# Kernel optimization log

Measured on AMD Instinct MI355X. Metric: run time of the kernel, lower is better.

The kernel has to match this reference:

```python
import jax, jax.numpy as jnp
import numpy as np

EPS = 1e-5
GROUPS = 32


def conv2d(x, w, b):
    # x: [N,C,H,W], w: [O,I,3,3] (or 1x1), stride 1, padding 'same' for 3x3
    kh = w.shape[2]
    pad = (kh - 1) // 2
    y = jax.lax.conv_general_dilated(x, w, (1, 1), ((pad, pad), (pad, pad)),
                                     dimension_numbers=('NCHW', 'OIHW', 'NCHW'))
    return y + b[None, :, None, None]


def group_norm(x, g, b):
    N, C, H, W = x.shape
    xr = x.reshape(N, GROUPS, C // GROUPS, H, W)
    mu = xr.mean(axis=(2, 3, 4), keepdims=True)
    var = xr.var(axis=(2, 3, 4), keepdims=True)
    xr = (xr - mu) / jnp.sqrt(var + EPS)
    return xr.reshape(N, C, H, W) * g[None, :, None, None] + b[None, :, None, None]


def batch_norm(x, g, b):
    # training-mode BatchNorm2d: batch statistics over (N,H,W)
    mu = x.mean(axis=(0, 2, 3), keepdims=True)
    var = x.var(axis=(0, 2, 3), keepdims=True)
    return (x - mu) / jnp.sqrt(var + EPS) * g[None, :, None, None] + b[None, :, None, None]


def binary_activation(x):
    # STE: forward sign(x), backward through piecewise poly out3
    out_fwd = jnp.sign(x)
    m1 = (x < -1).astype(x.dtype)
    m2 = (x < 0).astype(x.dtype)
    m3 = (x < 1).astype(x.dtype)
    out1 = -1.0 * m1 + (x * x + 2.0 * x) * (1.0 - m1)
    out2 = out1 * m2 + (-x * x + 2.0 * x) * (1.0 - m2)
    out3 = out2 * m3 + 1.0 * (1.0 - m3)
    return jax.lax.stop_gradient(out_fwd - out3) + out3


def hard_binary_conv(x, w, b):
    # per-output-channel scaling * sign(w), STE through clipped weights
    scale = jax.lax.stop_gradient(jnp.mean(jnp.abs(w), axis=(1, 2, 3), keepdims=True))
    bw_ng = scale * jnp.sign(w)
    clipped = jnp.clip(w, -1.0, 1.0)
    bw = jax.lax.stop_gradient(bw_ng - clipped) + clipped
    return conv2d(x, bw, b)


def learnable_bias(x, emb, w, b):
    bias = jax.nn.silu(emb) @ w.T + b  # [B, C]
    return x + bias[:, :, None, None]


def _forward(c, x, emb,
             rb_gn1_g, rb_gn1_b, rb_conv1_w, rb_conv1_b, rb_emb_w, rb_emb_b,
             rb_gn2_g, rb_gn2_b, rb_conv2_w, rb_conv2_b,
             m1_w, m1_b, bconv_w, bconv_b, bn_g, bn_b,
             m2_w, m2_b, prelu_a, m3_w, m3_b):
    # ResBlock (skip = Identity since out_channels == channels)
    h = conv2d(jax.nn.silu(group_norm(c, rb_gn1_g, rb_gn1_b)), rb_conv1_w, rb_conv1_b)
    eo = jax.nn.silu(emb) @ rb_emb_w.T + rb_emb_b          # [B, 2*C]
    scale, shift = jnp.split(eo[:, :, None, None], 2, axis=1)
    h = group_norm(h, rb_gn2_g, rb_gn2_b) * (1.0 + scale) + shift
    h = conv2d(jax.nn.silu(h), rb_conv2_w, rb_conv2_b)
    c2 = c + h
    # concat + bias + STE binarize + binary conv + BN + channel-pool residual + PReLU
    xc = jnp.concatenate([x, c2], axis=1)                   # [B, 2C, H, W]
    out = learnable_bias(xc, emb, m1_w, m1_b)
    out = binary_activation(out)
    out = hard_binary_conv(out, bconv_w, bconv_b)
    out = batch_norm(out, bn_g, bn_b)
    N, C2, H, W = xc.shape
    out = out + xc.reshape(N, C2 // 2, 2, H, W).mean(axis=2)  # channel mean pooling
    out = learnable_bias(out, emb, m2_w, m2_b)
    out = jnp.where(out >= 0, out, prelu_a[None, :, None, None] * out)  # PReLU
    out = learnable_bias(out, emb, m3_w, m3_b)
    return out


def setup_inputs() -> dict:
    key = jax.random.key(0)
    ks = jax.random.split(key, 24)
    B, C, EMB, H, W = 8, 128, 512, 64, 64
    IN2 = 2 * C
    n = lambda k, s, sc=0.05: jax.random.normal(k, s, dtype=jnp.float32) * sc
    return {
        'c': jax.random.normal(ks[0], (B, C, H, W), dtype=jnp.float32),
        'x': jax.random.normal(ks[1], (B, C, H, W), dtype=jnp.float32),
        'emb': jax.random.normal(ks[2], (B, EMB), dtype=jnp.float32),
        'rb_gn1_g': jnp.ones((C,), jnp.float32), 'rb_gn1_b': jnp.zeros((C,), jnp.float32),
        'rb_conv1_w': n(ks[3], (C, C, 3, 3)), 'rb_conv1_b': n(ks[4], (C,)),
        'rb_emb_w': n(ks[5], (2 * C, EMB)), 'rb_emb_b': n(ks[6], (2 * C,)),
        'rb_gn2_g': jnp.ones((C,), jnp.float32), 'rb_gn2_b': jnp.zeros((C,), jnp.float32),
        'rb_conv2_w': n(ks[7], (C, C, 3, 3)), 'rb_conv2_b': n(ks[8], (C,)),
        'm1_w': n(ks[9], (IN2, EMB)), 'm1_b': n(ks[10], (IN2,)),
        'bconv_w': jax.random.uniform(ks[11], (C, IN2, 3, 3), dtype=jnp.float32) * 0.001,
        'bconv_b': n(ks[12], (C,)),
        'bn_g': jnp.ones((C,), jnp.float32), 'bn_b': jnp.zeros((C,), jnp.float32),
        'm2_w': n(ks[13], (C, EMB)), 'm2_b': n(ks[14], (C,)),
        'prelu_a': jnp.full((C,), 0.25, jnp.float32),
        'm3_w': n(ks[15], (C, EMB)), 'm3_b': n(ks[16], (C,)),
    }


def reference(c, x, emb,
              rb_gn1_g, rb_gn1_b, rb_conv1_w, rb_conv1_b, rb_emb_w, rb_emb_b,
              rb_gn2_g, rb_gn2_b, rb_conv2_w, rb_conv2_b,
              m1_w, m1_b, bconv_w, bconv_b, bn_g, bn_b,
              m2_w, m2_b, prelu_a, m3_w, m3_b):
    return _forward(c, x, emb,
                    rb_gn1_g, rb_gn1_b, rb_conv1_w, rb_conv1_b, rb_emb_w, rb_emb_b,
                    rb_gn2_g, rb_gn2_b, rb_conv2_w, rb_conv2_b,
                    m1_w, m1_b, bconv_w, bconv_b, bn_g, bn_b,
                    m2_w, m2_b, prelu_a, m3_w, m3_b)
```

## Files before the change

### kernel.cpp

```cpp
#include <hip/hip_runtime.h>
#include <stdint.h>


#define B_   8
#define C_   128
#define C2_  256
#define HW_  4096
#define EMB_ 512
#define EPS_ 1e-5f

typedef int   v16i __attribute__((ext_vector_type(16)));
typedef float v16f __attribute__((ext_vector_type(16)));
typedef short v8s  __attribute__((ext_vector_type(8)));
typedef int   v4i  __attribute__((ext_vector_type(4)));

#define COLB 272
#define LDSZ (3 * 66 * COLB)
#define TSTRIDE 132

__device__ __forceinline__ float silu(float v) {
    return v * __builtin_amdgcn_rcpf(1.f + __expf(-v));
}
__device__ __forceinline__ unsigned short f2bf(float f) {
    unsigned int x = __float_as_uint(f);
    return (unsigned short)((x + 0x7FFFu + ((x >> 16) & 1u)) >> 16);
}
__device__ __forceinline__ int8_t sgn8(float v) {
    return (v > 0.f) ? (int8_t)1 : ((v < 0.f) ? (int8_t)(-1) : (int8_t)0);
}

__device__ __forceinline__ void stage_one(char* lds, int r, const char* src) {
    const int tid = threadIdx.x;
#pragma unroll
    for (int it = 0; it < 4; ++it) {
        int idx = it * 256 + tid;
        int x = idx >> 4, o = idx & 15;
        char* dst = lds + (r * 66 + x + 1) * COLB + o * 16;
        if (src) *(float4*)dst = *(const float4*)(src + x * 256 + o * 16);
        else     *(float4*)dst = make_float4(0.f, 0.f, 0.f, 0.f);
    }
}
__device__ __forceinline__ void stage3(char* lds, const char* r0,
                                       const char* r1, const char* r2) {
    const int tid = threadIdx.x;
    if (tid < 96) {
        int r = tid / 32, q = tid & 31;
        int c = (q >> 4) ? 65 : 0, o = q & 15;
        *(float4*)(lds + (r * 66 + c) * COLB + o * 16) = make_float4(0.f, 0.f, 0.f, 0.f);
    }
    stage_one(lds, 0, r0);
    stage_one(lds, 1, r1);
    stage_one(lds, 2, r2);
}

__global__ __launch_bounds__(256) void k_prep(
    const float* __restrict__ w, int8_t* __restrict__ sgn,
    float* __restrict__ alpha, float* __restrict__ bnS, float* __restrict__ bnQ,
    float* __restrict__ gnS, float* __restrict__ gnQ,
    const float* __restrict__ w1, const float* __restrict__ w2,
    unsigned short* __restrict__ Wc1, unsigned short* __restrict__ Wc2,
    const float* __restrict__ emb,
    const float* __restrict__ ew, const float* __restrict__ ebb,
    const float* __restrict__ m1w, const float* __restrict__ m1b,
    const float* __restrict__ m2w, const float* __restrict__ m2b,
    const float* __restrict__ m3w, const float* __restrict__ m3b,
    float* __restrict__ eo, float* __restrict__ b1,
    float* __restrict__ b2, float* __restrict__ b3,
    const float* __restrict__ gin, const float* __restrict__ g1w,
    const float* __restrict__ g1b, unsigned short* __restrict__ act1) {
    __shared__ float red[256];
    const int blk = blockIdx.x, tid = threadIdx.x;
    if (blk < 128) {
        const int o = blk;
        if (o == 0 && tid < 128) { bnS[tid] = 0.f; bnQ[tid] = 0.f; }
        if (o == 1) { gnS[tid] = 0.f; }
        if (o == 2) { gnQ[tid] = 0.f; }
        const float* wr = w + (size_t)o * (C2_ * 9);
        float s = 0.f;
        for (int i = tid; i < C2_ * 9; i += 256) s += fabsf(wr[i]);
        red[tid] = s;
        __syncthreads();
        for (int st = 128; st > 0; st >>= 1) {
            if (tid < st) red[tid] += red[tid + st];
            __syncthreads();
        }
        if (tid == 0) alpha[o] = red[0] / (float)(C2_ * 9);
        for (int kk = 0; kk < 9; ++kk) {
            float v = wr[tid * 9 + kk];
            sgn[((size_t)(kk * 16 + (tid >> 4)) * C_ + o) * 16 + (tid & 15)] = sgn8(v);
        }
    } else if (blk < 704) {
        int i = (blk - 128) * 256 + tid;
        int co = i / (C_ * 9);
        int rem = i - co * (C_ * 9);
        int ci = rem / 9, kk = rem - ci * 9;
        size_t d = ((size_t)(kk * 16 + (ci >> 3)) * C_ + co) * 8 + (ci & 7);
        Wc1[d] = f2bf(w1[i]);
        Wc2[d] = f2bf(w2[i]);
    } else if (blk < 896) {
        const int o = (blk - 704) * 4 + (tid >> 6);
        const int l = tid & 63;
        const float* wv;
        float bias;
        float* dst;
        int dstride;
        if (o < 256)      { wv = ew  + (size_t)o * EMB_;              bias = ebb[o];    dst = eo + o;  dstride = 256; }
        else if (o < 512) { int r = o - 256; wv = m1w + (size_t)r * EMB_; bias = m1b[r]; dst = b1 + r; dstride = 256; }
        else if (o < 640) { int r = o - 512; wv = m2w + (size_t)r * EMB_; bias = m2b[r]; dst = b2 + r; dstride = 128; }
        else              { int r = o - 640; wv = m3w + (size_t)r * EMB_; bias = m3b[r]; dst = b3 + r; dstride = 128; }
        const float4 wa = *(const float4*)(wv + 8 * l);
        const float4 wb = *(const float4*)(wv + 8 * l + 4);
#pragma unroll
        for (int b = 0; b < B_; ++b) {
            const float* s = emb + b * EMB_ + 8 * l;
            float4 sa = *(const float4*)(s);
            float4 sb = *(const float4*)(s + 4);
            float p = wa.x * silu(sa.x) + wa.y * silu(sa.y) + wa.z * silu(sa.z) + wa.w * silu(sa.w) +
                      wb.x * silu(sb.x) + wb.y * silu(sb.y) + wb.z * silu(sb.z) + wb.w * silu(sb.w);
#pragma unroll
            for (int off = 32; off > 0; off >>= 1) p += __shfl_down(p, off, 64);
            if (l == 0) dst[b * dstride] = bias + p;
        }
    } else {
        const int bb = blk - 896;
        const int n = bb >> 5, grp = bb & 31;
        const size_t base = ((size_t)(n * C_ + grp * 4)) << 12;
        float sum = 0.f, sq = 0.f;
        const float4* in4 = (const float4*)(gin + base);
        for (int i = tid; i < 4096; i += 256) {
            float4 v = in4[i];
            sum += v.x + v.y + v.z + v.w;
            sq += v.x * v.x + v.y * v.y + v.z * v.z + v.w * v.w;
        }
#pragma unroll
        for (int off = 32; off > 0; off >>= 1) {
            sum += __shfl_xor(sum, off, 64);
            sq  += __shfl_xor(sq, off, 64);
        }
        if ((tid & 63) == 0) { red[tid >> 6] = sum; red[8 + (tid >> 6)] = sq; }
        __syncthreads();
        sum = red[0] + red[1] + red[2] + red[3];
        sq  = red[8] + red[9] + red[10] + red[11];
        const float mu = sum * (1.f / 16384.f);
        const float rstd = rsqrtf(sq * (1.f / 16384.f) - mu * mu + EPS_);
        float gg[4], bb4[4];
#pragma unroll
        for (int j = 0; j < 4; ++j) { gg[j] = g1w[grp * 4 + j]; bb4[j] = g1b[grp * 4 + j]; }
        union F4 { float4 v; float f[4]; };
        for (int i = tid; i < 1024; i += 256) {
            const int hw = 4 * i;
            F4 vj[4];
#pragma unroll
            for (int j = 0; j < 4; ++j)
                vj[j].v = *(const float4*)(gin + base + ((size_t)j << 12) + hw);
#pragma unroll
            for (int e = 0; e < 4; ++e) {
                union { unsigned short u[4]; uint2 v; } pk;
#pragma unroll
                for (int j = 0; j < 4; ++j)
                    pk.u[j] = f2bf(silu((vj[j].f[e] - mu) * rstd * gg[j] + bb4[j]));
                *(uint2*)(act1 + ((size_t)(n * HW_ + hw + e)) * C_ + grp * 4) = pk.v;
            }
        }
    }
}

__global__ __launch_bounds__(256) void k_conv1(const unsigned short* __restrict__ act,
                                               const unsigned short* __restrict__ Wc,
                                               const float* __restrict__ bias,
                                               float* __restrict__ outN,
                                               float* __restrict__ gnS,
                                               float* __restrict__ gnQ) {
    __shared__ __align__(16) char lds[LDSZ];
    const int y = blockIdx.x;
    const int n = blockIdx.y;
    const char* base = (const char*)(act + ((size_t)n * 64) * 64 * C_);
    stage3(lds,
           (y > 0)  ? base + (size_t)(y - 1) * 16384 : nullptr,
           base + (size_t)y * 16384,
           (y < 63) ? base + (size_t)(y + 1) * 16384 : nullptr);
    __syncthreads();

    const int w = threadIdx.x >> 6;
    const int l = threadIdx.x & 63;
    const int lm = l & 31;
    const int lh = l >> 5;

    v16f acc0, acc1;
#pragma unroll
    for (int i = 0; i < 16; ++i) { acc0[i] = 0.f; acc1[i] = 0.f; }

#pragma unroll
    for (int kk = 0; kk < 9; ++kk) {
        const int r = kk / 3, dx = kk % 3 - 1;
        const char* col0 = lds + (r * 66 + lm + 1 + dx) * COLB + 16 * lh;
        const char* col1 = col0 + 32 * COLB;
        const unsigned short* wbase = Wc + (size_t)(kk * 16 + lh) * C_ * 8 + (32 * w + lm) * 8;
#pragma unroll
        for (int cb = 0; cb < 8; ++cb) {
            v8s a = *(const v8s*)(wbase + (size_t)(2 * cb) * C_ * 8);
            v8s b0 = *(const v8s*)(col0 + 32 * cb);
            v8s b1 = *(const v8s*)(col1 + 32 * cb);
            acc0 = __builtin_amdgcn_mfma_f32_32x32x16_bf16(a, b0, acc0, 0, 0, 0);
            acc1 = __builtin_amdgcn_mfma_f32_32x32x16_bf16(a, b1, acc1, 0, 0, 0);
        }
    }
    float sv0[16], sv1[16], pr[16], qr[16];
#pragma unroll
    for (int r = 0; r < 16; ++r) {
        const int row = (r & 3) + 8 * (r >> 2) + 4 * lh;
        const int co = 32 * w + row;
        const float bv = bias[co];
        float v0 = acc0[r] + bv, v1 = acc1[r] + bv;
        sv0[r] = v0;
        sv1[r] = v1;
        pr[r] = v0 + v1;
        qr[r] = v0 * v0 + v1 * v1;
    }
    __syncthreads();
    float* ldsT = (float*)lds;
    float* ldsS = (float*)(lds + 64 * TSTRIDE * 4);
    float* ldsQ = ldsS + 128;
#pragma unroll
    for (int r = 0; r < 16; ++r) {
        const int row = (r & 3) + 8 * (r >> 2) + 4 * lh;
        const int co = 32 * w + row;
        ldsT[lm * TSTRIDE + co] = sv0[r];
        ldsT[(32 + lm) * TSTRIDE + co] = sv1[r];
        float p = pr[r], q = qr[r];
#pragma unroll
        for (int m = 16; m > 0; m >>= 1) {
            p += __shfl_xor(p, m, 64);
            q += __shfl_xor(q, m, 64);
        }
        if (lm == 0) { ldsS[co] = p; ldsQ[co] = q; }
    }
    __syncthreads();
    if (threadIdx.x < 32) {
        const int g = threadIdx.x;
        float p = ldsS[4 * g] + ldsS[4 * g + 1] + ldsS[4 * g + 2] + ldsS[4 * g + 3];
        float q = ldsQ[4 * g] + ldsQ[4 * g + 1] + ldsQ[4 * g + 2] + ldsQ[4 * g + 3];
        atomicAdd(&gnS[n * 32 + g], p);
        atomicAdd(&gnQ[n * 32 + g], q);
    }
    const int q4 = threadIdx.x & 31;
    float* orow = outN + (((size_t)(n * HW_) + (y << 6)) << 7);
#pragma unroll
    for (int it = 0; it < 8; ++it) {
        const int px = it * 8 + (threadIdx.x >> 5);
        *(float4*)(orow + ((size_t)px << 7) + 4 * q4) =
            *(const float4*)(ldsT + px * TSTRIDE + 4 * q4);
    }
}

__global__ __launch_bounds__(256) void k_conv2(const float* __restrict__ yin,
                                               const unsigned short* __restrict__ Wc,
                                               const float* __restrict__ bias,
                                               const float* __restrict__ res,
                                               const float* __restrict__ xin,
                                               const float* __restrict__ b1v,
                                               const float* __restrict__ eo,
                                               const float* __restrict__ g2,
                                               const float* __restrict__ bt2,
                                               const float* __restrict__ gnS,
                                               const float* __restrict__ gnQ,
                                               float* __restrict__ poolC2,
                                               int8_t* __restrict__ S) {
    __shared__ __align__(16) char lds[LDSZ];
    __shared__ float ldsA[128], ldsB[128];
    const int y = blockIdx.x;
    const int n = blockIdx.y;
    const int tid = threadIdx.x;

    if (tid < 128) {
        const int ch = tid, grp = tid >> 2;
        const float mu = gnS[n * 32 + grp] * (1.f / 16384.f);
        const float var = gnQ[n * 32 + grp] * (1.f / 16384.f) - mu * mu;
        const float rstd = rsqrtf(var + EPS_);
        const float gg = g2[ch] * rstd;
        const float sc = 1.f + eo[n * 256 + ch];
        ldsA[ch] = gg * sc;
        ldsB[ch] = (bt2[ch] - mu * gg) * sc + eo[n * 256 + 128 + ch];
    }
    if (tid < 96) {
        int r = tid / 32, q = tid & 31;
        int cpad = (q >> 4) ? 65 : 0, o = q & 15;
        *(float4*)(lds + (r * 66 + cpad) * COLB + o * 16) = make_float4(0.f, 0.f, 0.f, 0.f);
    }
    __syncthreads();

    const int qc = tid & 31;
    float A0 = ldsA[4 * qc], A1 = ldsA[4 * qc + 1], A2 = ldsA[4 * qc + 2], A3 = ldsA[4 * qc + 3];
    float B0 = ldsB[4 * qc], B1 = ldsB[4 * qc + 1], B2 = ldsB[4 * qc + 2], B3 = ldsB[4 * qc + 3];
#pragma unroll
    for (int r = 0; r < 3; ++r) {
        const int yy = y - 1 + r;
        const float* ysrc = yin + (((size_t)(n * HW_) + yy * 64) << 7);
        const bool ok = (yy >= 0 && yy < 64);
#pragma unroll
        for (int it = 0; it < 8; ++it) {
            const int px = it * 8 + (tid >> 5);
            char* dst = lds + (r * 66 + px + 1) * COLB + qc * 8;
            if (ok) {
                float4 v = *(const float4*)(ysrc + ((size_t)px << 7) + 4 * qc);
                union { unsigned short u[4]; uint2 q; } pk;
                pk.u[0] = f2bf(silu(v.x * A0 + B0));
                pk.u[1] = f2bf(silu(v.y * A1 + B1));
                pk.u[2] = f2bf(silu(v.z * A2 + B2));
                pk.u[3] = f2bf(silu(v.w * A3 + B3));
                *(uint2*)dst = pk.q;
            } else {
                *(uint2*)dst = make_uint2(0u, 0u);
            }
        }
    }
    __syncthreads();

    const int w = tid >> 6;
    const int l = tid & 63;
    const int lm = l & 31;
    const int lh = l >> 5;

    v16f acc0, acc1;
#pragma unroll
    for (int i = 0; i < 16; ++i) { acc0[i] = 0.f; acc1[i] = 0.f; }

#pragma unroll
    for (int kk = 0; kk < 9; ++kk) {
        const int r = kk / 3, dx = kk % 3 - 1;
        const char* col0 = lds + (r * 66 + lm + 1 + dx) * COLB + 16 * lh;
        const char* col1 = col0 + 32 * COLB;
        const unsigned short* wbase = Wc + (size_t)(kk * 16 + lh) * C_ * 8 + (32 * w + lm) * 8;
#pragma unroll
        for (int cb = 0; cb < 8; ++cb) {
            v8s a = *(const v8s*)(wbase + (size_t)(2 * cb) * C_ * 8);
            v8s b0 = *(const v8s*)(col0 + 32 * cb);
            v8s b1 = *(const v8s*)(col1 + 32 * cb);
            acc0 = __builtin_amdgcn_mfma_f32_32x32x16_bf16(a, b0, acc0, 0, 0, 0);
            acc1 = __builtin_amdgcn_mfma_f32_32x32x16_bf16(a, b1, acc1, 0, 0, 0);
        }
    }
    float c2v0[16], c2v1[16];
#pragma unroll
    for (int r = 0; r < 16; ++r) {
        const int row = (r & 3) + 8 * (r >> 2) + 4 * lh;
        const int co = 32 * w + row;
        const float bv = bias[co];
        const size_t o = (((size_t)n * C_ + co) << 12) + (y << 6);
        c2v0[r] = acc0[r] + bv + res[o + lm];
        c2v1[r] = acc1[r] + bv + res[o + 32 + lm];
    }
#pragma unroll
    for (int q = 0; q < 4; ++q) {
        const int pc = 16 * w + 4 * q + 2 * lh;
        const size_t po = (((size_t)n * 64 + pc) << 12) + (y << 6);
        poolC2[po + lm]             = 0.5f * (c2v0[4 * q] + c2v0[4 * q + 1]);
        poolC2[po + 32 + lm]        = 0.5f * (c2v1[4 * q] + c2v1[4 * q + 1]);
        poolC2[po + 4096 + lm]      = 0.5f * (c2v0[4 * q + 2] + c2v0[4 * q + 3]);
        poolC2[po + 4096 + 32 + lm] = 0.5f * (c2v1[4 * q + 2] + c2v1[4 * q + 3]);
    }

    __syncthreads();
#pragma unroll
    for (int q = 0; q < 4; ++q) {
        const int co0 = 32 * w + 8 * q + 4 * lh;
        const float b0 = b1v[n * 256 + 128 + co0];
        const float b1b = b1v[n * 256 + 128 + co0 + 1];
        const float b2b = b1v[n * 256 + 128 + co0 + 2];
        const float b3b = b1v[n * 256 + 128 + co0 + 3];
        union { int8_t b[4]; int u; } p0, p1;
        p0.b[0] = sgn8(c2v0[4 * q] + b0);      p1.b[0] = sgn8(c2v1[4 * q] + b0);
        p0.b[1] = sgn8(c2v0[4 * q + 1] + b1b); p1.b[1] = sgn8(c2v1[4 * q + 1] + b1b);
        p0.b[2] = sgn8(c2v0[4 * q + 2] + b2b); p1.b[2] = sgn8(c2v1[4 * q + 2] + b2b);
        p0.b[3] = sgn8(c2v0[4 * q + 3] + b3b); p1.b[3] = sgn8(c2v1[4 * q + 3] + b3b);
        *(int*)(lds + lm * COLB + 128 + co0) = p0.u;
        *(int*)(lds + (32 + lm) * COLB + 128 + co0) = p1.u;
    }
#pragma unroll
    for (int u = 0; u < 8; ++u) {
        int idx = u * 256 + tid;
        int ch = idx >> 4, seg = idx & 15;
        float4 v = *(const float4*)(xin + (((size_t)(n * C_ + ch)) << 12) + (y << 6) + 4 * seg);
        const float bv = b1v[n * 256 + ch];
        lds[(4 * seg) * COLB + ch]     = sgn8(v.x + bv);
        lds[(4 * seg + 1) * COLB + ch] = sgn8(v.y + bv);
        lds[(4 * seg + 2) * COLB + ch] = sgn8(v.z + bv);
        lds[(4 * seg + 3) * COLB + ch] = sgn8(v.w + bv);
    }
    __syncthreads();
    int8_t* Srow = S + ((size_t)(n * HW_) + (y << 6)) * C2_;
#pragma unroll
    for (int u = 0; u < 4; ++u) {
        int idx = u * 256 + tid;
        int px = idx >> 4, c16 = idx & 15;
        *(int4*)(Srow + (size_t)px * C2_ + 16 * c16) = *(const int4*)(lds + px * COLB + 16 * c16);
    }
}

__global__ __launch_bounds__(256) void k_bconv(const int8_t* __restrict__ S,
                                               const int8_t* __restrict__ Wk,
                                               const float* __restrict__ alpha,
                                               const float* __restrict__ bias,
                                               float* __restrict__ out,
                                               float* __restrict__ bnS,
                                               float* __restrict__ bnQ) {
    __shared__ __align__(16) char lds[LDSZ];
    const int y = blockIdx.x;
    const int n = blockIdx.y;
    const char* base = (const char*)(S + ((size_t)n * 64) * 64 * C2_);
    stage3(lds,
           (y > 0)  ? base + (size_t)(y - 1) * 16384 : nullptr,
           base + (size_t)y * 16384,
           (y < 63) ? base + (size_t)(y + 1) * 16384 : nullptr);
    __syncthreads();

    const int w = threadIdx.x >> 6;
    const int l = threadIdx.x & 63;
    const int lm = l & 31;
    const int lh = l >> 5;

    v16i acc0, acc1;
#pragma unroll
    for (int i = 0; i < 16; ++i) { acc0[i] = 0; acc1[i] = 0; }

#pragma unroll
    for (int kk = 0; kk < 9; ++kk) {
        const int r = kk / 3, dx = kk % 3 - 1;
        const char* col0 = lds + (r * 66 + lm + 1 + dx) * COLB + 16 * lh;
        const char* col1 = col0 + 32 * COLB;
        const int8_t* wbase = Wk + (size_t)(kk * 16 + lh) * C_ * 16 + (32 * w + lm) * 16;
#pragma unroll
        for (int s = 0; s < 8; ++s) {
            v4i a = *(const v4i*)(wbase + (size_t)(2 * s) * C_ * 16);
            v4i b0 = *(const v4i*)(col0 + 32 * s);
            v4i b1 = *(const v4i*)(col1 + 32 * s);
            acc0 = __builtin_amdgcn_mfma_i32_32x32x32_i8(a, b0, acc0, 0, 0, 0);
            acc1 = __builtin_amdgcn_mfma_i32_32x32x32_i8(a, b1, acc1, 0, 0, 0);
        }
    }

    float pr[16], qr[16];
#pragma unroll
    for (int r = 0; r < 16; ++r) {
        const int row = (r & 3) + 8 * (r >> 2) + 4 * lh;
        const int co = 32 * w + row;
        const float av = alpha[co], bv = bias[co];
        const size_t o = (((size_t)n * C_ + co) << 12) + (y << 6);
        float v0 = av * (float)acc0[r] + bv;
        float v1 = av * (float)acc1[r] + bv;
        out[o + lm]      = v0;
        out[o + 32 + lm] = v1;
        pr[r] = v0 + v1;
        qr[r] = v0 * v0 + v1 * v1;
    }
    __syncthreads();
    float* ldsS = (float*)lds;
    float* ldsQ = (float*)lds + 128;
#pragma unroll
    for (int r = 0; r < 16; ++r) {
        float p = pr[r], q = qr[r];
#pragma unroll
        for (int m = 16; m > 0; m >>= 1) {
            p += __shfl_xor(p, m, 64);
            q += __shfl_xor(q, m, 64);
        }
        if (lm == 0) {
            const int row = (r & 3) + 8 * (r >> 2) + 4 * lh;
            const int co = 32 * w + row;
            ldsS[co] = p;
            ldsQ[co] = q;
        }
    }
    __syncthreads();
    if (threadIdx.x < 128) {
        atomicAdd(&bnS[threadIdx.x], ldsS[threadIdx.x]);
        atomicAdd(&bnQ[threadIdx.x], ldsQ[threadIdx.x]);
    }
}

__global__ __launch_bounds__(256) void k_final(const float* __restrict__ y3,
                                               const float* __restrict__ x,
                                               const float* __restrict__ poolC2,
                                               const float* __restrict__ bnS,
                                               const float* __restrict__ bnQ,
                                               const float* __restrict__ bng,
                                               const float* __restrict__ bnb,
                                               const float* __restrict__ b2v,
                                               const float* __restrict__ pa,
                                               const float* __restrict__ b3v,
                                               float* __restrict__ out) {
    const int idx4 = blockIdx.x * 256 + threadIdx.x;
    const int hw = (idx4 & 1023) * 4;
    const int cb = idx4 >> 10;
    const int co = cb & 127;
    const int n = cb >> 7;
    const float mu = bnS[co] * (1.f / 32768.f);
    const float var = bnQ[co] * (1.f / 32768.f) - mu * mu;
    const float rstd = rsqrtf(var + EPS_);
    const float gm = rstd * bng[co];
    const float bt = bnb[co] - mu * gm;
    const size_t obase = (((size_t)(n * C_ + co)) << 12) + hw;
    float4 v = *(const float4*)(y3 + obase);
    v.x = v.x * gm + bt; v.y = v.y * gm + bt; v.z = v.z * gm + bt; v.w = v.w * gm + bt;

    float4 pv;
    if (co < 64) {
        const int ch0 = 2 * co;
        float4 pA = *(const float4*)(x + (((size_t)(n * C_ + ch0)) << 12) + hw);
        float4 pB = *(const float4*)(x + (((size_t)(n * C_ + ch0 + 1)) << 12) + hw);
        pv.x = 0.5f * (pA.x + pB.x); pv.y = 0.5f * (pA.y + pB.y);
        pv.z = 0.5f * (pA.z + pB.z); pv.w = 0.5f * (pA.w + pB.w);
    } else {
        pv = *(const float4*)(poolC2 + (((size_t)(n * 64 + co - 64)) << 12) + hw);
    }
    const float bias2 = b2v[n * 128 + co];
    const float aP = pa[co];
    const float bias3 = b3v[n * 128 + co];
    float4 r;
    float t;
    t = v.x + pv.x + bias2; t = (t >= 0.f) ? t : aP * t; r.x = t + bias3;
    t = v.y + pv.y + bias2; t = (t >= 0.f) ? t : aP * t; r.y = t + bias3;
    t = v.z + pv.z + bias2; t = (t >= 0.f) ? t : aP * t; r.z = t + bias3;
    t = v.w + pv.w + bias2; t = (t >= 0.f) ? t : aP * t; r.w = t + bias3;
    *(float4*)(out + obase) = r;
}

extern "C" void kernel_launch(void* const* d_in, const int* in_sizes, int n_in,
                              void* d_out, int out_size, void* d_ws, size_t ws_size,
                              hipStream_t stream) {
    const float* c       = (const float*)d_in[0];
    const float* x       = (const float*)d_in[1];
    const float* emb     = (const float*)d_in[2];
    const float* gn1_g   = (const float*)d_in[3];
    const float* gn1_b   = (const float*)d_in[4];
    const float* conv1_w = (const float*)d_in[5];
    const float* conv1_b = (const float*)d_in[6];
    const float* emb_w   = (const float*)d_in[7];
    const float* emb_b   = (const float*)d_in[8];
    const float* gn2_g   = (const float*)d_in[9];
    const float* gn2_b   = (const float*)d_in[10];
    const float* conv2_w = (const float*)d_in[11];
    const float* conv2_b = (const float*)d_in[12];
    const float* m1_w    = (const float*)d_in[13];
    const float* m1_b    = (const float*)d_in[14];
    const float* bconv_w = (const float*)d_in[15];
    const float* bconv_b = (const float*)d_in[16];
    const float* bn_g    = (const float*)d_in[17];
    const float* bn_b    = (const float*)d_in[18];
    const float* m2_w    = (const float*)d_in[19];
    const float* m2_b    = (const float*)d_in[20];
    const float* prelu_a = (const float*)d_in[21];
    const float* m3_w    = (const float*)d_in[22];
    const float* m3_b    = (const float*)d_in[23];
    float* out = (float*)d_out;

    float* ws = (float*)d_ws;
    const size_t NCHW = (size_t)B_ * C_ * HW_;
    float*  poolC2 = ws;
    float*  y_buf = ws + NCHW;
    unsigned short* actA = (unsigned short*)(ws + 2 * NCHW);
    int8_t* S     = (int8_t*)(ws + 2 * NCHW);
    int8_t* sgn   = (int8_t*)(ws + 2 * NCHW + NCHW / 2);
    unsigned short* Wc1 = (unsigned short*)(ws + 2 * NCHW + NCHW / 2 + 73728);
    unsigned short* Wc2 = Wc1 + C_ * C_ * 9;
    float*  alpha = ws + 2 * NCHW + NCHW / 2 + 73728 + 2 * 73728;
    float*  eo    = alpha + 128;
    float*  b1v   = eo + B_ * 256;
    float*  b2v   = b1v + B_ * 256;
    float*  b3v   = b2v + B_ * 128;
    float*  bnS   = b3v + B_ * 128;
    float*  bnQ   = bnS + 128;
    float*  gnS   = bnQ + 128;
    float*  gnQ   = gnS + 256;

    k_prep<<<1152, 256, 0, stream>>>(bconv_w, sgn, alpha, bnS, bnQ, gnS, gnQ,
                                     conv1_w, conv2_w, Wc1, Wc2,
                                     emb, emb_w, emb_b, m1_w, m1_b, m2_w, m2_b,
                                     m3_w, m3_b, eo, b1v, b2v, b3v,
                                     c, gn1_g, gn1_b, actA);
    k_conv1<<<dim3(64, B_), 256, 0, stream>>>(actA, Wc1, conv1_b, y_buf, gnS, gnQ);
    k_conv2<<<dim3(64, B_), 256, 0, stream>>>(y_buf, Wc2, conv2_b, c, x, b1v, eo,
                                              gn2_g, gn2_b, gnS, gnQ, poolC2, S);
    k_bconv<<<dim3(64, B_), 256, 0, stream>>>(S, sgn, alpha, bconv_b, y_buf, bnS, bnQ);
    k_final<<<NCHW / 1024, 256, 0, stream>>>(y_buf, x, poolC2, bnS, bnQ, bn_g, bn_b,
                                             b2v, prelu_a, b3v, out);
}
```

Measured before the change: 242.7 us.

## Fuse GroupNorm1+SiLU into conv1 staging and split conv kernels to 512 threads

```diff
diff --git a/kernel.cpp b/kernel.cpp
--- a/kernel.cpp
+++ b/kernel.cpp
@@ -27,30 +27,6 @@
 }
 __device__ __forceinline__ int8_t sgn8(float v) {
     return (v > 0.f) ? (int8_t)1 : ((v < 0.f) ? (int8_t)(-1) : (int8_t)0);
-}
-
-__device__ __forceinline__ void stage_one(char* lds, int r, const char* src) {
-    const int tid = threadIdx.x;
-#pragma unroll
-    for (int it = 0; it < 4; ++it) {
-        int idx = it * 256 + tid;
-        int x = idx >> 4, o = idx & 15;
-        char* dst = lds + (r * 66 + x + 1) * COLB + o * 16;
-        if (src) *(float4*)dst = *(const float4*)(src + x * 256 + o * 16);
-        else     *(float4*)dst = make_float4(0.f, 0.f, 0.f, 0.f);
-    }
-}
-__device__ __forceinline__ void stage3(char* lds, const char* r0,
-                                       const char* r1, const char* r2) {
-    const int tid = threadIdx.x;
-    if (tid < 96) {
-        int r = tid / 32, q = tid & 31;
-        int c = (q >> 4) ? 65 : 0, o = q & 15;
-        *(float4*)(lds + (r * 66 + c) * COLB + o * 16) = make_float4(0.f, 0.f, 0.f, 0.f);
-    }
-    stage_one(lds, 0, r0);
-    stage_one(lds, 1, r1);
-    stage_one(lds, 2, r2);
 }
 
 __global__ __launch_bounds__(256) void k_prep(
@@ -66,8 +42,8 @@
     const float* __restrict__ m3w, const float* __restrict__ m3b,
     float* __restrict__ eo, float* __restrict__ b1,
     float* __restrict__ b2, float* __restrict__ b3,
-    const float* __restrict__ gin, const float* __restrict__ g1w,
-    const float* __restrict__ g1b, unsigned short* __restrict__ act1) {
+    const float* __restrict__ gin,
+    float* __restrict__ g1S, float* __restrict__ g1Q) {
     __shared__ float red[256];
     const int blk = blockIdx.x, tid = threadIdx.x;
     if (blk < 128) {
@@ -139,133 +115,141 @@
         }
         if ((tid & 63) == 0) { red[tid >> 6] = sum; red[8 + (tid >> 6)] = sq; }
         __syncthreads();
-        sum = red[0] + red[1] + red[2] + red[3];
-        sq  = red[8] + red[9] + red[10] + red[11];
-        const float mu = sum * (1.f / 16384.f);
-        const float rstd = rsqrtf(sq * (1.f / 16384.f) - mu * mu + EPS_);
-        float gg[4], bb4[4];
-#pragma unroll
-        for (int j = 0; j < 4; ++j) { gg[j] = g1w[grp * 4 + j]; bb4[j] = g1b[grp * 4 + j]; }
-        union F4 { float4 v; float f[4]; };
-        for (int i = tid; i < 1024; i += 256) {
-            const int hw = 4 * i;
-            F4 vj[4];
-#pragma unroll
-            for (int j = 0; j < 4; ++j)
-                vj[j].v = *(const float4*)(gin + base + ((size_t)j << 12) + hw);
-#pragma unroll
-            for (int e = 0; e < 4; ++e) {
-                union { unsigned short u[4]; uint2 v; } pk;
-#pragma unroll
-                for (int j = 0; j < 4; ++j)
-                    pk.u[j] = f2bf(silu((vj[j].f[e] - mu) * rstd * gg[j] + bb4[j]));
-                *(uint2*)(act1 + ((size_t)(n * HW_ + hw + e)) * C_ + grp * 4) = pk.v;
-            }
-        }
-    }
-}
-
-__global__ __launch_bounds__(256) void k_conv1(const unsigned short* __restrict__ act,
-                                               const unsigned short* __restrict__ Wc,
-                                               const float* __restrict__ bias,
-                                               float* __restrict__ outN,
-                                               float* __restrict__ gnS,
-                                               float* __restrict__ gnQ) {
+        if (tid == 0) {
+            g1S[n * 32 + grp] = red[0] + red[1] + red[2] + red[3];
+            g1Q[n * 32 + grp] = red[8] + red[9] + red[10] + red[11];
+        }
+    }
+}
+
+__global__ __launch_bounds__(512, 4) void k_conv1(
+    const float* __restrict__ cin,
+    const unsigned short* __restrict__ Wc,
+    const float* __restrict__ bias,
+    const float* __restrict__ g1w, const float* __restrict__ g1b,
+    const float* __restrict__ g1S, const float* __restrict__ g1Q,
+    float* __restrict__ outN,
+    float* __restrict__ gnS, float* __restrict__ gnQ) {
     __shared__ __align__(16) char lds[LDSZ];
+    __shared__ float chA[128], chB[128];
     const int y = blockIdx.x;
     const int n = blockIdx.y;
-    const char* base = (const char*)(act + ((size_t)n * 64) * 64 * C_);
-    stage3(lds,
-           (y > 0)  ? base + (size_t)(y - 1) * 16384 : nullptr,
-           base + (size_t)y * 16384,
-           (y < 63) ? base + (size_t)(y + 1) * 16384 : nullptr);
-    __syncthreads();
-
-    const int w = threadIdx.x >> 6;
-    const int l = threadIdx.x & 63;
+    const int tid = threadIdx.x;
+
+    if (tid < 128) {
+        const int ch = tid, grp = tid >> 2;
+        const float mu = g1S[n * 32 + grp] * (1.f / 16384.f);
+        const float var = g1Q[n * 32 + grp] * (1.f / 16384.f) - mu * mu;
+        const float rstd = rsqrtf(var + EPS_);
+        const float A = g1w[ch] * rstd;
+        chA[ch] = A;
+        chB[ch] = g1b[ch] - mu * A;
+    }
+    if (tid < 96) {
+        int r = tid / 32, q = tid & 31;
+        int c = (q >> 4) ? 65 : 0, o = q & 15;
+        *(float4*)(lds + (r * 66 + c) * COLB + o * 16) = make_float4(0.f, 0.f, 0.f, 0.f);
+    }
+    __syncthreads();
+
+#pragma unroll
+    for (int u = 0; u < 12; ++u) {
+        int unit = u * 512 + tid;
+        int r = unit >> 11, rem = unit & 2047;
+        int ch = rem >> 4, seg = rem & 15;
+        int yy = y - 1 + r;
+        char* dst = lds + (r * 66 + 1 + seg) * COLB + 2 * ch;
+        if (yy >= 0 && yy < 64) {
+            const float A = chA[ch], Bv = chB[ch];
+            const float* src = cin + (((size_t)(n * C_ + ch)) << 12) + yy * 64 + seg;
+#pragma unroll
+            for (int j = 0; j < 4; ++j)
+                *(unsigned short*)(dst + (16 * j) * COLB) = f2bf(silu(src[16 * j] * A + Bv));
+        } else {
+#pragma unroll
+            for (int j = 0; j < 4; ++j)
+                *(unsigned short*)(dst + (16 * j) * COLB) = 0;
+        }
+    }
+    __syncthreads();
+
+    const int w = tid >> 6;
+    const int og = w >> 1;
+    const int ph = w & 1;
+    const int l = tid & 63;
     const int lm = l & 31;
     const int lh = l >> 5;
 
-    v16f acc0, acc1;
-#pragma unroll
-    for (int i = 0; i < 16; ++i) { acc0[i] = 0.f; acc1[i] = 0.f; }
+    v16f acc;
+#pragma unroll
+    for (int i = 0; i < 16; ++i) acc[i] = 0.f;
 
 #pragma unroll
     for (int kk = 0; kk < 9; ++kk) {
         const int r = kk / 3, dx = kk % 3 - 1;
-        const char* col0 = lds + (r * 66 + lm + 1 + dx) * COLB + 16 * lh;
-        const char* col1 = col0 + 32 * COLB;
-        const unsigned short* wbase = Wc + (size_t)(kk * 16 + lh) * C_ * 8 + (32 * w + lm) * 8;
+        const char* col = lds + (r * 66 + 32 * ph + lm + 1 + dx) * COLB + 16 * lh;
+        const unsigned short* wbase = Wc + (size_t)(kk * 16 + lh) * C_ * 8 + (32 * og + lm) * 8;
 #pragma unroll
         for (int cb = 0; cb < 8; ++cb) {
             v8s a = *(const v8s*)(wbase + (size_t)(2 * cb) * C_ * 8);
-            v8s b0 = *(const v8s*)(col0 + 32 * cb);
-            v8s b1 = *(const v8s*)(col1 + 32 * cb);
-            acc0 = __builtin_amdgcn_mfma_f32_32x32x16_bf16(a, b0, acc0, 0, 0, 0);
-            acc1 = __builtin_amdgcn_mfma_f32_32x32x16_bf16(a, b1, acc1, 0, 0, 0);
-        }
-    }
-    float sv0[16], sv1[16], pr[16], qr[16];
+            v8s b = *(const v8s*)(col + 32 * cb);
+            acc = __builtin_amdgcn_mfma_f32_32x32x16_bf16(a, b, acc, 0, 0, 0);
+        }
+    }
+    __syncthreads();
+    float* ldsT = (float*)lds;
+    float* ldsS = (float*)(lds + 64 * TSTRIDE * 4);
+    float* ldsQ = ldsS + 256;
 #pragma unroll
     for (int r = 0; r < 16; ++r) {
         const int row = (r & 3) + 8 * (r >> 2) + 4 * lh;
-        const int co = 32 * w + row;
-        const float bv = bias[co];
-        float v0 = acc0[r] + bv, v1 = acc1[r] + bv;
-        sv0[r] = v0;
-        sv1[r] = v1;
-        pr[r] = v0 + v1;
-        qr[r] = v0 * v0 + v1 * v1;
-    }
-    __syncthreads();
-    float* ldsT = (float*)lds;
-    float* ldsS = (float*)(lds + 64 * TSTRIDE * 4);
-    float* ldsQ = ldsS + 128;
-#pragma unroll
-    for (int r = 0; r < 16; ++r) {
-        const int row = (r & 3) + 8 * (r >> 2) + 4 * lh;
-        const int co = 32 * w + row;
-        ldsT[lm * TSTRIDE + co] = sv0[r];
-        ldsT[(32 + lm) * TSTRIDE + co] = sv1[r];
-        float p = pr[r], q = qr[r];
+        const int co = 32 * og + row;
+        float v = acc[r] + bias[co];
+        ldsT[(32 * ph + lm) * TSTRIDE + co] = v;
+        float p = v, q = v * v;
 #pragma unroll
         for (int m = 16; m > 0; m >>= 1) {
             p += __shfl_xor(p, m, 64);
             q += __shfl_xor(q, m, 64);
         }
-        if (lm == 0) { ldsS[co] = p; ldsQ[co] = q; }
-    }
-    __syncthreads();
-    if (threadIdx.x < 32) {
-        const int g = threadIdx.x;
-        float p = ldsS[4 * g] + ldsS[4 * g + 1] + ldsS[4 * g + 2] + ldsS[4 * g + 3];
-        float q = ldsQ[4 * g] + ldsQ[4 * g + 1] + ldsQ[4 * g + 2] + ldsQ[4 * g + 3];
+        if (lm == 0) { ldsS[ph * 128 + co] = p; ldsQ[ph * 128 + co] = q; }
+    }
+    __syncthreads();
+    if (tid < 32) {
+        const int g = tid;
+        float p = 0.f, q = 0.f;
+#pragma unroll
+        for (int j = 0; j < 4; ++j) {
+            p += ldsS[4 * g + j] + ldsS[128 + 4 * g + j];
+            q += ldsQ[4 * g + j] + ldsQ[128 + 4 * g + j];
+        }
         atomicAdd(&gnS[n * 32 + g], p);
         atomicAdd(&gnQ[n * 32 + g], q);
     }
-    const int q4 = threadIdx.x & 31;
+    const int q4 = tid & 31;
     float* orow = outN + (((size_t)(n * HW_) + (y << 6)) << 7);
 #pragma unroll
-    for (int it = 0; it < 8; ++it) {
-        const int px = it * 8 + (threadIdx.x >> 5);
+    for (int it = 0; it < 4; ++it) {
+        const int px = it * 16 + (tid >> 5);
         *(float4*)(orow + ((size_t)px << 7) + 4 * q4) =
             *(const float4*)(ldsT + px * TSTRIDE + 4 * q4);
     }
 }
 
-__global__ __launch_bounds__(256) void k_conv2(const float* __restrict__ yin,
-                                               const unsigned short* __restrict__ Wc,
-                                               const float* __restrict__ bias,
-                                               const float* __restrict__ res,
-                                               const float* __restrict__ xin,
-                                               const float* __restrict__ b1v,
-                                               const float* __restrict__ eo,
-                                               const float* __restrict__ g2,
-                                               const float* __restrict__ bt2,
-                                               const float* __restrict__ gnS,
-                                               const float* __restrict__ gnQ,
-                                               float* __restrict__ poolC2,
-                                               int8_t* __restrict__ S) {
+__global__ __launch_bounds__(512, 4) void k_conv2(
+    const float* __restrict__ yin,
+    const unsigned short* __restrict__ Wc,
+    const float* __restrict__ bias,
+    const float* __restrict__ res,
+    const float* __restrict__ xin,
+    const float* __restrict__ b1v,
+    const float* __restrict__ eo,
+    const float* __restrict__ g2,
+    const float* __restrict__ bt2,
+    const float* __restrict__ gnS,
+    const float* __restrict__ gnQ,
+    float* __restrict__ poolC2,
+    int8_t* __restrict__ S) {
     __shared__ __align__(16) char lds[LDSZ];
     __shared__ float ldsA[128], ldsB[128];
     const int y = blockIdx.x;
@@ -290,16 +274,16 @@
     __syncthreads();
 
     const int qc = tid & 31;
-    float A0 = ldsA[4 * qc], A1 = ldsA[4 * qc + 1], A2 = ldsA[4 * qc + 2], A3 = ldsA[4 * qc + 3];
-    float B0 = ldsB[4 * qc], B1 = ldsB[4 * qc + 1], B2 = ldsB[4 * qc + 2], B3 = ldsB[4 * qc + 3];
+    const float A0 = ldsA[4 * qc], A1 = ldsA[4 * qc + 1], A2 = ldsA[4 * qc + 2], A3 = ldsA[4 * qc + 3];
+    const float B0 = ldsB[4 * qc], B1 = ldsB[4 * qc + 1], B2 = ldsB[4 * qc + 2], B3 = ldsB[4 * qc + 3];
 #pragma unroll
     for (int r = 0; r < 3; ++r) {
         const int yy = y - 1 + r;
         const float* ysrc = yin + (((size_t)(n * HW_) + yy * 64) << 7);
         const bool ok = (yy >= 0 && yy < 64);
 #pragma unroll
-        for (int it = 0; it < 8; ++it) {
-            const int px = it * 8 + (tid >> 5);
+        for (int it = 0; it < 4; ++it) {
+            const int px = it * 16 + (tid >> 5);
             char* dst = lds + (r * 66 + px + 1) * COLB + qc * 8;
             if (ok) {
                 float4 v = *(const float4*)(ysrc + ((size_t)px << 7) + 4 * qc);
@@ -317,68 +301,62 @@
     __syncthreads();
 
     const int w = tid >> 6;
+    const int og = w >> 1;
+    const int ph = w & 1;
     const int l = tid & 63;
     const int lm = l & 31;
     const int lh = l >> 5;
 
-    v16f acc0, acc1;
-#pragma unroll
-    for (int i = 0; i < 16; ++i) { acc0[i] = 0.f; acc1[i] = 0.f; }
+    v16f acc;
+#pragma unroll
+    for (int i = 0; i < 16; ++i) acc[i] = 0.f;
 
 #pragma unroll
     for (int kk = 0; kk < 9; ++kk) {
         const int r = kk / 3, dx = kk % 3 - 1;
-        const char* col0 = lds + (r * 66 + lm + 1 + dx) * COLB + 16 * lh;
-        const char* col1 = col0 + 32 * COLB;
-        const unsigned short* wbase = Wc + (size_t)(kk * 16 + lh) * C_ * 8 + (32 * w + lm) * 8;
+        const char* col = lds + (r * 66 + 32 * ph + lm + 1 + dx) * COLB + 16 * lh;
+        const unsigned short* wbase = Wc + (size_t)(kk * 16 + lh) * C_ * 8 + (32 * og + lm) * 8;
 #pragma unroll
         for (int cb = 0; cb < 8; ++cb) {
             v8s a = *(const v8s*)(wbase + (size_t)(2 * cb) * C_ * 8);
-            v8s b0 = *(const v8s*)(col0 + 32 * cb);
-            v8s b1 = *(const v8s*)(col1 + 32 * cb);
-            acc0 = __builtin_amdgcn_mfma_f32_32x32x16_bf16(a, b0, acc0, 0, 0, 0);
-            acc1 = __builtin_amdgcn_mfma_f32_32x32x16_bf16(a, b1, acc1, 0, 0, 0);
-        }
-    }
-    float c2v0[16], c2v1[16];
+            v8s b = *(const v8s*)(col + 32 * cb);
+            acc = __builtin_amdgcn_mfma_f32_32x32x16_bf16(a, b, acc, 0, 0, 0);
+        }
+    }
+    float c2v[16];
 #pragma unroll
     for (int r = 0; r < 16; ++r) {
         const int row = (r & 3) + 8 * (r >> 2) + 4 * lh;
-        const int co = 32 * w + row;
-        const float bv = bias[co];
+        const int co = 32 * og + row;
         const size_t o = (((size_t)n * C_ + co) << 12) + (y << 6);
-        c2v0[r] = acc0[r] + bv + res[o + lm];
-        c2v1[r] = acc1[r] + bv + res[o + 32 + lm];
+        c2v[r] = acc[r] + bias[co] + res[o + 32 * ph + lm];
     }
 #pragma unroll
     for (int q = 0; q < 4; ++q) {
-        const int pc = 16 * w + 4 * q + 2 * lh;
+        const int pc = 16 * og + 4 * q + 2 * lh;
         const size_t po = (((size_t)n * 64 + pc) << 12) + (y << 6);
-        poolC2[po + lm]             = 0.5f * (c2v0[4 * q] + c2v0[4 * q + 1]);
-        poolC2[po + 32 + lm]        = 0.5f * (c2v1[4 * q] + c2v1[4 * q + 1]);
-        poolC2[po + 4096 + lm]      = 0.5f * (c2v0[4 * q + 2] + c2v0[4 * q + 3]);
-        poolC2[po + 4096 + 32 + lm] = 0.5f * (c2v1[4 * q + 2] + c2v1[4 * q + 3]);
+        poolC2[po + 32 * ph + lm]        = 0.5f * (c2v[4 * q] + c2v[4 * q + 1]);
+        poolC2[po + 4096 + 32 * ph + lm] = 0.5f * (c2v[4 * q + 2] + c2v[4 * q + 3]);
     }
 
     __syncthreads();
 #pragma unroll
     for (int q = 0; q < 4; ++q) {
-        const int co0 = 32 * w + 8 * q + 4 * lh;
+        const int co0 = 32 * og + 8 * q + 4 * lh;
         const float b0 = b1v[n * 256 + 128 + co0];
         const float b1b = b1v[n * 256 + 128 + co0 + 1];
         const float b2b = b1v[n * 256 + 128 + co0 + 2];
         const float b3b = b1v[n * 256 + 128 + co0 + 3];
-        union { int8_t b[4]; int u; } p0, p1;
-        p0.b[0] = sgn8(c2v0[4 * q] + b0);      p1.b[0] = sgn8(c2v1[4 * q] + b0);
-        p0.b[1] = sgn8(c2v0[4 * q + 1] + b1b); p1.b[1] = sgn8(c2v1[4 * q + 1] + b1b);
-        p0.b[2] = sgn8(c2v0[4 * q + 2] + b2b); p1.b[2] = sgn8(c2v1[4 * q + 2] + b2b);
-        p0.b[3] = sgn8(c2v0[4 * q + 3] + b3b); p1.b[3] = sgn8(c2v1[4 * q + 3] + b3b);
-        *(int*)(lds + lm * COLB + 128 + co0) = p0.u;
-        *(int*)(lds + (32 + lm) * COLB + 128 + co0) = p1.u;
-    }
-#pragma unroll
-    for (int u = 0; u < 8; ++u) {
-        int idx = u * 256 + tid;
+        union { int8_t b[4]; int u; } p0;
+        p0.b[0] = sgn8(c2v[4 * q] + b0);
+        p0.b[1] = sgn8(c2v[4 * q + 1] + b1b);
+        p0.b[2] = sgn8(c2v[4 * q + 2] + b2b);
+        p0.b[3] = sgn8(c2v[4 * q + 3] + b3b);
+        *(int*)(lds + (32 * ph + lm) * COLB + 128 + co0) = p0.u;
+    }
+#pragma unroll
+    for (int u = 0; u < 4; ++u) {
+        int idx = u * 512 + tid;
         int ch = idx >> 4, seg = idx & 15;
         float4 v = *(const float4*)(xin + (((size_t)(n * C_ + ch)) << 12) + (y << 6) + 4 * seg);
         const float bv = b1v[n * 256 + ch];
@@ -390,91 +368,97 @@
     __syncthreads();
     int8_t* Srow = S + ((size_t)(n * HW_) + (y << 6)) * C2_;
 #pragma unroll
-    for (int u = 0; u < 4; ++u) {
-        int idx = u * 256 + tid;
+    for (int u = 0; u < 2; ++u) {
+        int idx = u * 512 + tid;
         int px = idx >> 4, c16 = idx & 15;
         *(int4*)(Srow + (size_t)px * C2_ + 16 * c16) = *(const int4*)(lds + px * COLB + 16 * c16);
     }
 }
 
-__global__ __launch_bounds__(256) void k_bconv(const int8_t* __restrict__ S,
-                                               const int8_t* __restrict__ Wk,
-                                               const float* __restrict__ alpha,
-                                               const float* __restrict__ bias,
-                                               float* __restrict__ out,
-                                               float* __restrict__ bnS,
-                                               float* __restrict__ bnQ) {
+__global__ __launch_bounds__(512, 4) void k_bconv(
+    const int8_t* __restrict__ S,
+    const int8_t* __restrict__ Wk,
+    const float* __restrict__ alpha,
+    const float* __restrict__ bias,
+    float* __restrict__ out,
+    float* __restrict__ bnS, float* __restrict__ bnQ) {
     __shared__ __align__(16) char lds[LDSZ];
     const int y = blockIdx.x;
     const int n = blockIdx.y;
+    const int tid = threadIdx.x;
     const char* base = (const char*)(S + ((size_t)n * 64) * 64 * C2_);
-    stage3(lds,
-           (y > 0)  ? base + (size_t)(y - 1) * 16384 : nullptr,
-           base + (size_t)y * 16384,
-           (y < 63) ? base + (size_t)(y + 1) * 16384 : nullptr);
-    __syncthreads();
-
-    const int w = threadIdx.x >> 6;
-    const int l = threadIdx.x & 63;
+    const char* r0 = (y > 0)  ? base + (size_t)(y - 1) * 16384 : nullptr;
+    const char* r1 = base + (size_t)y * 16384;
+    const char* r2 = (y < 63) ? base + (size_t)(y + 1) * 16384 : nullptr;
+    if (tid < 96) {
+        int r = tid / 32, q = tid & 31;
+        int c = (q >> 4) ? 65 : 0, o = q & 15;
+        *(float4*)(lds + (r * 66 + c) * COLB + o * 16) = make_float4(0.f, 0.f, 0.f, 0.f);
+    }
+    {
+        const char* rs0 = r0; const char* rs1 = r1; const char* rs2 = r2;
+#pragma unroll
+        for (int it = 0; it < 2; ++it) {
+            int idx = it * 512 + tid;
+            int x = idx >> 4, o = idx & 15;
+            char* d0 = lds + (0 * 66 + x + 1) * COLB + o * 16;
+            char* d1 = lds + (1 * 66 + x + 1) * COLB + o * 16;
+            char* d2 = lds + (2 * 66 + x + 1) * COLB + o * 16;
+            if (rs0) *(float4*)d0 = *(const float4*)(rs0 + x * 256 + o * 16);
+            else     *(float4*)d0 = make_float4(0.f, 0.f, 0.f, 0.f);
+            *(float4*)d1 = *(const float4*)(rs1 + x * 256 + o * 16);
+            if (rs2) *(float4*)d2 = *(const float4*)(rs2 + x * 256 + o * 16);
+            else     *(float4*)d2 = make_float4(0.f, 0.f, 0.f, 0.f);
+        }
+    }
+    __syncthreads();
+
+    const int w = tid >> 6;
+    const int og = w >> 1;
+    const int ph = w & 1;
+    const int l = tid & 63;
     const int lm = l & 31;
     const int lh = l >> 5;
 
-    v16i acc0, acc1;
-#pragma unroll
-    for (int i = 0; i < 16; ++i) { acc0[i] = 0; acc1[i] = 0; }
+    v16i acc;
+#pragma unroll
+    for (int i = 0; i < 16; ++i) acc[i] = 0;
 
 #pragma unroll
     for (int kk = 0; kk < 9; ++kk) {
         const int r = kk / 3, dx = kk % 3 - 1;
-        const char* col0 = lds + (r * 66 + lm + 1 + dx) * COLB + 16 * lh;
-        const char* col1 = col0 + 32 * COLB;
-        const int8_t* wbase = Wk + (size_t)(kk * 16 + lh) * C_ * 16 + (32 * w + lm) * 16;
+        const char* col = lds + (r * 66 + 32 * ph + lm + 1 + dx) * COLB + 16 * lh;
+        const int8_t* wbase = Wk + (size_t)(kk * 16 + lh) * C_ * 16 + (32 * og + lm) * 16;
 #pragma unroll
         for (int s = 0; s < 8; ++s) {
             v4i a = *(const v4i*)(wbase + (size_t)(2 * s) * C_ * 16);
-            v4i b0 = *(const v4i*)(col0 + 32 * s);
-            v4i b1 = *(const v4i*)(col1 + 32 * s);
-            acc0 = __builtin_amdgcn_mfma_i32_32x32x32_i8(a, b0, acc0, 0, 0, 0);
-            acc1 = __builtin_amdgcn_mfma_i32_32x32x32_i8(a, b1, acc1, 0, 0, 0);
-        }
-    }
-
-    float pr[16], qr[16];
+            v4i b = *(const v4i*)(col + 32 * s);
+            acc = __builtin_amdgcn_mfma_i32_32x32x32_i8(a, b, acc, 0, 0, 0);
+        }
+    }
+    __syncthreads();
+    float* ldsS = (float*)lds;
+    float* ldsQ = (float*)lds + 256;
 #pragma unroll
     for (int r = 0; r < 16; ++r) {
         const int row = (r & 3) + 8 * (r >> 2) + 4 * lh;
-        const int co = 32 * w + row;
+        const int co = 32 * og + row;
         const float av = alpha[co], bv = bias[co];
         const size_t o = (((size_t)n * C_ + co) << 12) + (y << 6);
-        float v0 = av * (float)acc0[r] + bv;
-        float v1 = av * (float)acc1[r] + bv;
-        out[o + lm]      = v0;
-        out[o + 32 + lm] = v1;
-        pr[r] = v0 + v1;
-        qr[r] = v0 * v0 + v1 * v1;
-    }
-    __syncthreads();
-    float* ldsS = (float*)lds;
-    float* ldsQ = (float*)lds + 128;
-#pragma unroll
-    for (int r = 0; r < 16; ++r) {
-        float p = pr[r], q = qr[r];
+        float v = av * (float)acc[r] + bv;
+        out[o + 32 * ph + lm] = v;
+        float p = v, q = v * v;
 #pragma unroll
         for (int m = 16; m > 0; m >>= 1) {
             p += __shfl_xor(p, m, 64);
             q += __shfl_xor(q, m, 64);
         }
-        if (lm == 0) {
-            const int row = (r & 3) + 8 * (r >> 2) + 4 * lh;
-            const int co = 32 * w + row;
-            ldsS[co] = p;
-            ldsQ[co] = q;
-        }
-    }
-    __syncthreads();
-    if (threadIdx.x < 128) {
-        atomicAdd(&bnS[threadIdx.x], ldsS[threadIdx.x]);
-        atomicAdd(&bnQ[threadIdx.x], ldsQ[threadIdx.x]);
+        if (lm == 0) { ldsS[ph * 128 + co] = p; ldsQ[ph * 128 + co] = q; }
+    }
+    __syncthreads();
+    if (tid < 128) {
+        atomicAdd(&bnS[tid], ldsS[tid] + ldsS[128 + tid]);
+        atomicAdd(&bnQ[tid], ldsQ[tid] + ldsQ[128 + tid]);
     }
 }
 
@@ -558,7 +542,6 @@
     const size_t NCHW = (size_t)B_ * C_ * HW_;
     float*  poolC2 = ws;
     float*  y_buf = ws + NCHW;
-    unsigned short* actA = (unsigned short*)(ws + 2 * NCHW);
     int8_t* S     = (int8_t*)(ws + 2 * NCHW);
     int8_t* sgn   = (int8_t*)(ws + 2 * NCHW + NCHW / 2);
     unsigned short* Wc1 = (unsigned short*)(ws + 2 * NCHW + NCHW / 2 + 73728);
@@ -572,16 +555,19 @@
     float*  bnQ   = bnS + 128;
     float*  gnS   = bnQ + 128;
     float*  gnQ   = gnS + 256;
+    float*  g1S   = gnQ + 256;
+    float*  g1Q   = g1S + 256;
 
     k_prep<<<1152, 256, 0, stream>>>(bconv_w, sgn, alpha, bnS, bnQ, gnS, gnQ,
                                      conv1_w, conv2_w, Wc1, Wc2,
                                      emb, emb_w, emb_b, m1_w, m1_b, m2_w, m2_b,
                                      m3_w, m3_b, eo, b1v, b2v, b3v,
-                                     c, gn1_g, gn1_b, actA);
-    k_conv1<<<dim3(64, B_), 256, 0, stream>>>(actA, Wc1, conv1_b, y_buf, gnS, gnQ);
-    k_conv2<<<dim3(64, B_), 256, 0, stream>>>(y_buf, Wc2, conv2_b, c, x, b1v, eo,
+                                     c, g1S, g1Q);
+    k_conv1<<<dim3(64, B_), 512, 0, stream>>>(c, Wc1, conv1_b, gn1_g, gn1_b,
+                                              g1S, g1Q, y_buf, gnS, gnQ);
+    k_conv2<<<dim3(64, B_), 512, 0, stream>>>(y_buf, Wc2, conv2_b, c, x, b1v, eo,
                                               gn2_g, gn2_b, gnS, gnQ, poolC2, S);
-    k_bconv<<<dim3(64, B_), 256, 0, stream>>>(S, sgn, alpha, bconv_b, y_buf, bnS, bnQ);
+    k_bconv<<<dim3(64, B_), 512, 0, stream>>>(S, sgn, alpha, bconv_b, y_buf, bnS, bnQ);
     k_final<<<NCHW / 1024, 256, 0, stream>>>(y_buf, x, poolC2, bnS, bnQ, bn_g, bn_b,
                                              b2v, prelu_a, b3v, out);
 }
```

Result: faster. 219.3 us (-9.6%).
